# Performance work log

Measured on AMD Instinct MI355X. Metric: run time of the kernel, lower is better.

Reference implementation:

```python
import jax, jax.numpy as jnp
import numpy as np

B, N, D, HEAD = 16, 1024, 512, 256  # hidden_size=512, gcn_layer=2 -> head_dim=256


def _xavier(key, shape):
    lim = (6.0 / (shape[0] + shape[-1])) ** 0.5
    return jax.random.uniform(key, shape, jnp.float32, -lim, lim)


def setup_inputs() -> dict:
    key = jax.random.key(0)
    ks = jax.random.split(key, 10)
    fi_lim = (6.0 / (D + 1)) ** 0.5
    return {
        "x": jax.random.normal(ks[0], (B, N, D), jnp.float32),
        "tp_w": _xavier(ks[1], (D, D)), "tp_b": jnp.zeros((D,), jnp.float32),
        "tc_w": _xavier(ks[2], (D, D)), "tc_b": jnp.zeros((D,), jnp.float32),
        "fi_w": jax.random.uniform(ks[3], (D,), jnp.float32, -fi_lim, fi_lim),
        "bil_w": _xavier(ks[4], (D, D)),
        "gcn_w0": _xavier(ks[5], (D, HEAD)), "gcn_b0": jnp.zeros((HEAD,), jnp.float32),
        "gcn_w1": _xavier(ks[6], (D + HEAD, HEAD)), "gcn_b1": jnp.zeros((HEAD,), jnp.float32),
        "out_w": _xavier(ks[7], (D, D)), "out_b": jnp.zeros((D,), jnp.float32),
    }


def reference(x, tp_w, tp_b, tc_w, tc_b, fi_w, bil_w,
              gcn_w0, gcn_b0, gcn_w1, gcn_b1, out_w, out_b):
    Bb, Nn, Dd = x.shape
    # ---- StructInduction: matrix-tree latent structure ----
    tp = jnp.tanh(x @ tp_w + tp_b)                      # [B,N,D]
    tc = jnp.tanh(x @ tc_w + tc_b)                      # [B,N,D]
    # original expands BOTH tp and tc along dim 2 -> f_ij[b,i,j] = s[b,i]
    s = jnp.einsum('bnd,de,bne->bn', tp, bil_w, tc)     # [B,N]
    f_i = jnp.exp(x @ fi_w)                             # [B,N] root scores
    eye = jnp.eye(Nn, dtype=x.dtype)
    A = jnp.exp(s)[:, :, None] * (1.0 - eye)            # [B,N,N], zero diagonal
    col_sum = A.sum(axis=1)                             # [B,N] sum over dim 1
    L = -A + col_sum[:, None, :] * eye                  # Laplacian
    L = L.at[:, 0, :].set(f_i)                          # replace row 0 with root scores
    Linv = jnp.linalg.inv(L)                            # [B,N,N]
    d0 = f_i * Linv[:, :, 0]                            # [B,N]
    diag = jnp.diagonal(Linv, axis1=-2, axis2=-1)       # [B,N]
    tmp1 = A * diag[:, None, :]                         # A[b,i,j]*Linv_diag[b,j]
    tmp2 = A * jnp.swapaxes(Linv, 1, 2)                 # A[b,i,j]*Linv[b,j,i]
    mask1 = jnp.concatenate([jnp.zeros((Nn, 1), x.dtype),
                             jnp.ones((Nn, Nn - 1), x.dtype)], axis=1)  # zero col 0
    mask2 = mask1.T                                     # zero row 0
    dx = mask1 * tmp1 - mask2 * tmp2                    # [B,N,N]
    d = jnp.concatenate([d0[:, None, :], dx], axis=1)   # [B,N+1,N]
    df = jnp.swapaxes(d, 1, 2)                          # [B,N,N+1]
    adj = df[:, :, 1:]                                  # [B,N,N] latent adjacency
    # ---- GraphConvLayer (self_loop=True, dropout = identity / eval) ----
    denom = adj.sum(axis=2, keepdims=True) + 1.0        # [B,N,1]
    outputs = x
    cache = [x]
    outs = []
    for (W, b) in ((gcn_w0, gcn_b0), (gcn_w1, gcn_b1)):
        Ax = adj @ outputs                              # [B,N,in_dim]
        AxW = (Ax @ W + b) + (outputs @ W + b)          # neighbor + self loop
        g = jax.nn.relu(AxW / denom)                    # [B,N,HEAD]
        cache.append(g)
        outputs = jnp.concatenate(cache, axis=2)        # densely connected
        outs.append(g)
    gcn_out = jnp.concatenate(outs, axis=2) + x         # [B,N,D] residual
    return gcn_out @ out_w + out_b
```

## Files before the change

### kernel.cpp

```cpp
#include <hip/hip_runtime.h>
#include <cmath>

#define BN   16384
#define DD   512
#define HEADN 256

typedef unsigned short ushort;
typedef short short8 __attribute__((ext_vector_type(8)));
typedef float floatx4 __attribute__((ext_vector_type(4)));
typedef unsigned short ushort4v __attribute__((ext_vector_type(4)));
typedef unsigned short ushort8v __attribute__((ext_vector_type(8)));

__device__ __forceinline__ ushort f2bf(float v) {
    unsigned int u = __float_as_uint(v);
    unsigned int r = u + 0x7FFFu + ((u >> 16) & 1u);
    return (ushort)(r >> 16);
}
__device__ __forceinline__ float bf2f(ushort u) {
    return __uint_as_float(((unsigned int)u) << 16);
}
__device__ __forceinline__ float tanh_fast(float x) {
    float xc = fminf(fmaxf(x, -15.0f), 15.0f);
    float e = __expf(2.0f * xc);
    return (e - 1.0f) * __builtin_amdgcn_rcpf(e + 1.0f);
}

template <int TM, int TN, int KK, int EPI>
__global__ __launch_bounds__(256) void gemm_lds(
    const ushort* __restrict__ A, int lda,
    const ushort* __restrict__ Bt, int N,
    const float* __restrict__ bias,
    const float* __restrict__ denom,
    const ushort* __restrict__ tcb, int tcld,
    float* __restrict__ s_arr,
    void* __restrict__ Cout, int ldc,
    const ushort* __restrict__ xgb, int xoff, ushort* __restrict__ gout)
{
    constexpr int MI = TM / 32;
    constexpr int NI = TN / 32;
    constexpr int ROWS = TM + TN;
    constexpr int CPT = (ROWS * 8) / 256;
    constexpr int MT = 16384 / TM;
    constexpr int MT_PER_BAND = MT / 8;
    constexpr int NK = KK >> 6;
    static_assert(NK >= 2, "need >=2 K-iters for depth-2 pipeline");
    static_assert(CPT == 6, "vmcnt literal below assumes CPT==6");
    __shared__ ushort S[3 * ROWS * 64];

    const int g = blockIdx.x;
    const int band = g & 7, within = g >> 3;
    const int nt = within / MT_PER_BAND;
    const int mt = band * MT_PER_BAND + (within - nt * MT_PER_BAND);
    const int m0 = mt * TM, n0 = nt * TN;
    const int w = threadIdx.x >> 6, L = threadIdx.x & 63;
    const int wr0 = (w >> 1) * (TM / 2), wc0 = (w & 1) * (TN / 2);
    const int lrow = L & 15, quad = L >> 4;

    const ushort* gbase[CPT];
#pragma unroll
    for (int rr = 0; rr < CPT; ++rr) {
        const int chunk = rr * 256 + (w << 6) + L;
        const int row = chunk >> 3, slot = chunk & 7;
        const int ca = slot ^ ((row >> 1) & 7);
        gbase[rr] = (row < TM)
            ? A  + (size_t)(m0 + row) * lda    + (ca << 3)
            : Bt + (size_t)(n0 + row - TM) * KK + (ca << 3);
    }

    floatx4 zero4 = {0.0f, 0.0f, 0.0f, 0.0f};
    floatx4 acc[MI][NI];
#pragma unroll
    for (int i = 0; i < MI; ++i)
#pragma unroll
        for (int j = 0; j < NI; ++j) acc[i][j] = zero4;

    auto stage = [&](int buf, int k0) {
        ushort* Sd = S + buf * (ROWS * 64);
#pragma unroll
        for (int rr = 0; rr < CPT; ++rr) {
            __builtin_amdgcn_global_load_lds(
                (const __attribute__((address_space(1))) unsigned int*)(gbase[rr] + k0),
                (__attribute__((address_space(3))) unsigned int*)(Sd + (rr * 256 + (w << 6)) * 8),
                16, 0, 0);
        }
    };

    stage(0, 0);
    stage(1, 64);
#pragma unroll
    for (int kk = 0; kk < NK; ++kk) {
        if (kk + 1 < NK) {
            asm volatile("s_waitcnt vmcnt(6) lgkmcnt(0)" ::: "memory");
            __builtin_amdgcn_s_barrier();
            __builtin_amdgcn_sched_barrier(0);
        } else {
            __syncthreads();
        }
        if (kk + 2 < NK) stage((kk + 2) % 3, (kk + 2) << 6);

        const ushort* Sc = S + (kk % 3) * (ROWS * 64);
        short8 af[2][MI], bfr[2][NI];
#pragma unroll
        for (int ks = 0; ks < 2; ++ks) {
#pragma unroll
            for (int mi = 0; mi < MI; ++mi) {
                const int row = wr0 + (mi << 4) + lrow;
                const int slot = ((ks << 2) + quad) ^ ((row >> 1) & 7);
                af[ks][mi] = *(const short8*)(Sc + row * 64 + (slot << 3));
            }
#pragma unroll
            for (int ni = 0; ni < NI; ++ni) {
                const int row = TM + wc0 + (ni << 4) + lrow;
                const int slot = ((ks << 2) + quad) ^ ((row >> 1) & 7);
                bfr[ks][ni] = *(const short8*)(Sc + row * 64 + (slot << 3));
            }
        }
#pragma unroll
        for (int ks = 0; ks < 2; ++ks)
#pragma unroll
            for (int mi = 0; mi < MI; ++mi)
#pragma unroll
                for (int ni = 0; ni < NI; ++ni)
                    acc[mi][ni] = __builtin_amdgcn_mfma_f32_16x16x32_bf16(
                        bfr[ks][ni], af[ks][mi], acc[mi][ni], 0, 0, 0);
    }

    if constexpr (EPI == 3) {
#pragma unroll
        for (int mi = 0; mi < MI; ++mi) {
            const int gr = m0 + wr0 + (mi << 4) + lrow;
            float rs = 0.0f;
#pragma unroll
            for (int ni = 0; ni < NI; ++ni) {
                const int gcb = n0 + wc0 + (ni << 4) + (quad << 2);
                ushort4v t4 = *(const ushort4v*)(tcb + (size_t)gr * tcld + gcb);
#pragma unroll
                for (int p = 0; p < 4; ++p) rs += acc[mi][ni][p] * bf2f(t4[p]);
            }
            rs += __shfl_xor(rs, 16);
            rs += __shfl_xor(rs, 32);
            if (quad == 0) atomicAdd(s_arr + gr, rs);
        }
    } else {
#pragma unroll
        for (int mi = 0; mi < MI; ++mi) {
            const int gr = m0 + wr0 + (mi << 4) + lrow;
            const float rdv = (EPI == 2) ? __builtin_amdgcn_rcpf(denom[gr]) : 1.0f;
#pragma unroll
            for (int ni = 0; ni < NI; ++ni) {
                const int gcb = n0 + wc0 + (ni << 4) + (quad << 2);
                const floatx4 v = acc[mi][ni];
                if constexpr (EPI == 0) {
                    float4 bv = *(const float4*)(bias + gcb);
                    float4 o = {v[0] + bv.x, v[1] + bv.y, v[2] + bv.z, v[3] + bv.w};
                    *(float4*)((float*)Cout + (size_t)gr * ldc + gcb) = o;
                } else if constexpr (EPI == 1) {
                    float4 bv = *(const float4*)(bias + gcb);
                    ushort4v o;
                    o[0] = f2bf(tanh_fast(v[0] + bv.x));
                    o[1] = f2bf(tanh_fast(v[1] + bv.y));
                    o[2] = f2bf(tanh_fast(v[2] + bv.z));
                    o[3] = f2bf(tanh_fast(v[3] + bv.w));
                    *(ushort4v*)((ushort*)Cout + (size_t)gr * ldc + gcb) = o;
                } else {
                    float4 bv = *(const float4*)(bias + gcb);
                    float u0 = (v[0] + 2.0f * bv.x) * rdv; u0 = u0 > 0.0f ? u0 : 0.0f;
                    float u1 = (v[1] + 2.0f * bv.y) * rdv; u1 = u1 > 0.0f ? u1 : 0.0f;
                    float u2 = (v[2] + 2.0f * bv.z) * rdv; u2 = u2 > 0.0f ? u2 : 0.0f;
                    float u3 = (v[3] + 2.0f * bv.w) * rdv; u3 = u3 > 0.0f ? u3 : 0.0f;
                    if (Cout) {
                        ushort4v o;
                        o[0] = f2bf(u0); o[1] = f2bf(u1); o[2] = f2bf(u2); o[3] = f2bf(u3);
                        *(ushort4v*)((ushort*)Cout + (size_t)gr * ldc + gcb) = o;
                    }
                    if (gout) {
                        const size_t gb = (size_t)gr * 512 + xoff + gcb;
                        ushort4v xg = *(const ushort4v*)(xgb + gb);
                        ushort4v o;
                        o[0] = f2bf(u0 + bf2f(xg[0]));
                        o[1] = f2bf(u1 + bf2f(xg[1]));
                        o[2] = f2bf(u2 + bf2f(xg[2]));
                        o[3] = f2bf(u3 + bf2f(xg[3]));
                        *(ushort4v*)(gout + gb) = o;
                    }
                }
            }
        }
    }
}

__global__ __launch_bounds__(256) void prep_k(
    const float* __restrict__ x, const float* __restrict__ fiw,
    ushort* __restrict__ xb, float* __restrict__ fdot,
    const float* __restrict__ tp_w, const float* __restrict__ tc_w,
    const float* __restrict__ bilw, const float* __restrict__ ow,
    const float* __restrict__ w0, const float* __restrict__ w1,
    const float* __restrict__ tp_b, const float* __restrict__ tc_b,
    ushort* __restrict__ tptcwT, ushort* __restrict__ bilwT,
    ushort* __restrict__ owT, ushort* __restrict__ w0T,
    ushort* __restrict__ w1T, float* __restrict__ bias2,
    float* __restrict__ zstats, int zcount)
{
    const int blk0 = blockIdx.x;
    if (blk0 < 4096) {
        const int wv = threadIdx.x >> 6, L = threadIdx.x & 63;
        const int r = (blk0 << 2) + wv;
        const float* xr = x + (size_t)r * DD;
        const int c0 = L << 3;
        float4 v0 = *(const float4*)(xr + c0);
        float4 v1 = *(const float4*)(xr + c0 + 4);
        float4 f0 = *(const float4*)(fiw + c0);
        float4 f1 = *(const float4*)(fiw + c0 + 4);
        float d = v0.x * f0.x + v0.y * f0.y + v0.z * f0.z + v0.w * f0.w
                + v1.x * f1.x + v1.y * f1.y + v1.z * f1.z + v1.w * f1.w;
        ushort8v o;
        o[0] = f2bf(v0.x); o[1] = f2bf(v0.y); o[2] = f2bf(v0.z); o[3] = f2bf(v0.w);
        o[4] = f2bf(v1.x); o[5] = f2bf(v1.y); o[6] = f2bf(v1.z); o[7] = f2bf(v1.w);
        *(ushort8v*)(xb + (size_t)r * DD + c0) = o;
#pragma unroll
        for (int off = 32; off > 0; off >>= 1) d += __shfl_xor(d, off);
        if (L == 0) fdot[r] = d;
        return;
    }
    if (blk0 >= 5441) {
        for (int i = (blk0 - 5441) * 256 + threadIdx.x; i < zcount; i += 16 * 256)
            zstats[i] = 0.0f;
        return;
    }
    const int blk = blk0 - 4096;
    if (blk >= 1344) {
        for (int i = threadIdx.x; i < 512; i += 256) {
            bias2[i] = tp_b[i];
            bias2[512 + i] = tc_b[i];
        }
        return;
    }
    const float* W; ushort* Wt; int K, N, local;
    if (blk < 256)       { W = tp_w; Wt = tptcwT;              K = 512; N = 512; local = blk; }
    else if (blk < 512)  { W = tc_w; Wt = tptcwT + 512 * 512;  K = 512; N = 512; local = blk - 256; }
    else if (blk < 768)  { W = bilw; Wt = bilwT;               K = 512; N = 512; local = blk - 512; }
    else if (blk < 1024) { W = ow;   Wt = owT;                 K = 512; N = 512; local = blk - 768; }
    else if (blk < 1152) { W = w0;   Wt = w0T;                 K = 512; N = 256; local = blk - 1024; }
    else                 { W = w1;   Wt = w1T;                 K = 768; N = 256; local = blk - 1152; }

    __shared__ float t[32][33];
    const int nb = N >> 5;
    const int kb = local / nb, nbb = local % nb;
    const int k0 = kb << 5, n0 = nbb << 5;
    const int c = threadIdx.x & 31, r = threadIdx.x >> 5;
#pragma unroll
    for (int i = 0; i < 4; ++i)
        t[r + 8 * i][c] = W[(size_t)(k0 + r + 8 * i) * N + n0 + c];
    __syncthreads();
#pragma unroll
    for (int i = 0; i < 4; ++i)
        Wt[(size_t)(n0 + r + 8 * i) * K + k0 + c] = f2bf(t[c][r + 8 * i]);
}

__global__ __launch_bounds__(1024) void finalize_k(
    const float* __restrict__ s_arr, const float* __restrict__ fdot,
    float* __restrict__ a, float* __restrict__ f,
    float* __restrict__ Sb, float* __restrict__ Hb, float* __restrict__ den)
{
    __shared__ float redS[16], redH[16];
    __shared__ float Hsh;
    const int b = blockIdx.x, t = threadIdx.x;
    const int r = (b << 10) + t;
    const float av = __expf(s_arr[r]), fv = __expf(fdot[r]);
    a[r] = av; f[r] = fv;
    float s1 = av, s2 = av * fv;
#pragma unroll
    for (int o = 32; o > 0; o >>= 1) { s1 += __shfl_xor(s1, o); s2 += __shfl_xor(s2, o); }
    if ((t & 63) == 0) { redS[t >> 6] = s1; redH[t >> 6] = s2; }
    __syncthreads();
    if (t == 0) {
        float S = 0.f, H = 0.f;
        for (int i = 0; i < 16; ++i) { S += redS[i]; H += redH[i]; }
        Sb[b] = S; Hb[b] = H; Hsh = H;
    }
    __syncthreads();
    den[r] = 2.0f - av * fv * __builtin_amdgcn_rcpf(Hsh);
}

__global__ __launch_bounds__(256) void batch_pq(
    const ushort* __restrict__ V, const float* __restrict__ a, const float* __restrict__ f,
    float* __restrict__ P, float* __restrict__ Q, int C)
{
    __shared__ float redP[256][4];
    __shared__ float redQ[256][4];
    const int b = blockIdx.x >> 4;
    const int chunk = blockIdx.x & 15;
    const int c4cnt = C >> 2;
    const int rg = 256 / c4cnt;
    const int c4 = threadIdx.x & (c4cnt - 1);
    const int sub = threadIdx.x / c4cnt;
    const ushort* Vb = V + (size_t)b * 1024 * C;
    const float* ab = a + (b << 10);
    const float* fb = f + (b << 10);
    const int n0 = chunk << 6;
    float4 p = {0, 0, 0, 0}, q = {0, 0, 0, 0};
    for (int n = n0 + sub; n < n0 + 64; n += rg) {
        const float av = ab[n], afv = av * fb[n];
        ushort4v u = *(const ushort4v*)(Vb + (size_t)n * C + (c4 << 2));
        float4 v = {bf2f(u[0]), bf2f(u[1]), bf2f(u[2]), bf2f(u[3])};
        p.x += av * v.x; p.y += av * v.y; p.z += av * v.z; p.w += av * v.w;
        q.x += afv * v.x; q.y += afv * v.y; q.z += afv * v.z; q.w += afv * v.w;
    }
    redP[threadIdx.x][0] = p.x; redP[threadIdx.x][1] = p.y;
    redP[threadIdx.x][2] = p.z; redP[threadIdx.x][3] = p.w;
    redQ[threadIdx.x][0] = q.x; redQ[threadIdx.x][1] = q.y;
    redQ[threadIdx.x][2] = q.z; redQ[threadIdx.x][3] = q.w;
    __syncthreads();
    if (sub == 0) {
        for (int s = 1; s < rg; ++s) {
            const int t2 = threadIdx.x + s * c4cnt;
            p.x += redP[t2][0]; p.y += redP[t2][1]; p.z += redP[t2][2]; p.w += redP[t2][3];
            q.x += redQ[t2][0]; q.y += redQ[t2][1]; q.z += redQ[t2][2]; q.w += redQ[t2][3];
        }
        float* Pp = P + b * C + (c4 << 2);
        float* Qp = Q + b * C + (c4 << 2);
        atomicAdd(Pp + 0, p.x); atomicAdd(Pp + 1, p.y);
        atomicAdd(Pp + 2, p.z); atomicAdd(Pp + 3, p.w);
        atomicAdd(Qp + 0, q.x); atomicAdd(Qp + 1, q.y);
        atomicAdd(Qp + 2, q.z); atomicAdd(Qp + 3, q.w);
    }
}

__global__ __launch_bounds__(256) void mix_k(
    const ushort* __restrict__ V, const float* __restrict__ P, const float* __restrict__ Q,
    const float* __restrict__ a, const float* __restrict__ f,
    const float* __restrict__ Sb, const float* __restrict__ Hb,
    ushort* __restrict__ outb, int C, int ldo, int co)
{
    const int idx = blockIdx.x * 256 + threadIdx.x;
    const int c4c = C >> 2;
    const int r = idx / c4c, c4 = idx - r * c4c;
    const int b = r >> 10;
    const float av = a[r], fv = f[r], S = Sb[b], H = Hb[b];
    const float rS = __builtin_amdgcn_rcpf(S);
    const float beta = av * rS * __builtin_amdgcn_rcpf(H);
    const float alpha = 1.0f - av * rS;
    const float cp = rS - beta * fv;
    ushort4v u = *(const ushort4v*)(V + (size_t)r * C + (c4 << 2));
    float4 v = {bf2f(u[0]), bf2f(u[1]), bf2f(u[2]), bf2f(u[3])};
    const float* Pp = P + b * C + (c4 << 2);
    const float* Qp = Q + b * C + (c4 << 2);
    ushort4v o;
    o[0] = f2bf(alpha * v.x + cp * Pp[0] + beta * Qp[0]);
    o[1] = f2bf(alpha * v.y + cp * Pp[1] + beta * Qp[1]);
    o[2] = f2bf(alpha * v.z + cp * Pp[2] + beta * Qp[2]);
    o[3] = f2bf(alpha * v.w + cp * Pp[3] + beta * Qp[3]);
    *(ushort4v*)(outb + (size_t)r * ldo + co + (c4 << 2)) = o;
}

extern "C" void kernel_launch(void* const* d_in, const int* in_sizes, int n_in,
                              void* d_out, int out_size, void* d_ws, size_t ws_size,
                              hipStream_t stream)
{
    (void)in_sizes; (void)n_in; (void)out_size; (void)ws_size;
    const float* x    = (const float*)d_in[0];
    const float* tp_w = (const float*)d_in[1];
    const float* tp_b = (const float*)d_in[2];
    const float* tc_w = (const float*)d_in[3];
    const float* tc_b = (const float*)d_in[4];
    const float* fi_w = (const float*)d_in[5];
    const float* bilw = (const float*)d_in[6];
    const float* w0   = (const float*)d_in[7];
    const float* b0   = (const float*)d_in[8];
    const float* w1   = (const float*)d_in[9];
    const float* b1   = (const float*)d_in[10];
    const float* ow   = (const float*)d_in[11];
    const float* ob   = (const float*)d_in[12];

    char* W = (char*)d_ws;
    ushort* xb    = (ushort*)W;
    ushort* gcnb  = xb;
    ushort* tptcb = (ushort*)(W + ((size_t)16 << 20));
    ushort* Hbuf  = tptcb;
    ushort* g0b   = (ushort*)(W + ((size_t)48 << 20));
    ushort* tptcwT= (ushort*)(W + ((size_t)56 << 20));
    ushort* bilwT = tptcwT + 524288;
    ushort* owT   = bilwT + 262144;
    ushort* w0T   = owT + 262144;
    ushort* w1T   = w0T + 131072;
    float*  bias2 = (float*)(w1T + 196608);
    float* stats  = (float*)(W + ((size_t)60 << 20));
    float* s_arr  = stats;
    float* P0     = s_arr + 16384;
    float* Q0     = P0 + 8192;
    float* P1     = Q0 + 8192;
    float* Q1     = P1 + 4096;
    const int zcount = 16384 + 2 * 8192 + 2 * 4096;
    float* fdot   = Q1 + 4096;
    float* arr_a  = fdot + BN;
    float* arr_f  = arr_a + BN;
    float* arr_den= arr_f + BN;
    float* Sb     = arr_den + BN;
    float* Hb     = Sb + 16;

    prep_k<<<5457, 256, 0, stream>>>(x, fi_w, xb, fdot, tp_w, tc_w, bilw, ow, w0, w1,
                                     tp_b, tc_b, tptcwT, bilwT, owT, w0T, w1T, bias2,
                                     s_arr, zcount);
    gemm_lds<128, 64, 512, 1><<<2048, 256, 0, stream>>>(xb, 512, tptcwT, 1024, bias2,
        nullptr, nullptr, 0, nullptr, tptcb, 1024, nullptr, 0, nullptr);
    gemm_lds<128, 64, 512, 3><<<1024, 256, 0, stream>>>(tptcb, 1024, bilwT, 512, nullptr,
        nullptr, tptcb + 512, 1024, s_arr, nullptr, 0, nullptr, 0, nullptr);
    finalize_k<<<16, 1024, 0, stream>>>(s_arr, fdot, arr_a, arr_f, Sb, Hb, arr_den);
    batch_pq<<<256, 256, 0, stream>>>(xb, arr_a, arr_f, P0, Q0, 512);
    mix_k<<<8192, 256, 0, stream>>>(xb, P0, Q0, arr_a, arr_f, Sb, Hb, Hbuf, 512, 768, 0);
    gemm_lds<128, 64, 512, 2><<<512, 256, 0, stream>>>(Hbuf, 768, w0T, 256, b0,
        arr_den, nullptr, 0, nullptr, g0b, 256, xb, 0, gcnb);
    batch_pq<<<256, 256, 0, stream>>>(g0b, arr_a, arr_f, P1, Q1, 256);
    mix_k<<<4096, 256, 0, stream>>>(g0b, P1, Q1, arr_a, arr_f, Sb, Hb, Hbuf, 256, 768, 512);
    gemm_lds<128, 64, 768, 2><<<512, 256, 0, stream>>>(Hbuf, 768, w1T, 256, b1,
        arr_den, nullptr, 0, nullptr, nullptr, 0, xb, 256, gcnb);
    gemm_lds<128, 64, 512, 0><<<1024, 256, 0, stream>>>(gcnb, 512, owT, 512, ob,
        nullptr, nullptr, 0, nullptr, (float*)d_out, 512, nullptr, 0, nullptr);
}
```

Before: 230.8 us.

## Fuse finalize into batch_pq and fold layer-1 P/Q reduction into GEMM epilogue

Removes the separate finalize kernel by computing exp of scores, per-batch sums S and H (via atomics) inside the first batch-reduction kernel, and computing the denominator in the mix kernel. The second batch_pq launch is eliminated by accumulating the weighted column sums P1/Q1 directly in the layer-0 GEMM epilogue with shuffle reductions and atomics. This cuts two launches and a re-read of g0b, at the cost of extra atomics and register pressure in the GEMM epilogue and slight numeric differences from summing unrounded values.

After: 236.7 us. 1.03x slower.

```diff
diff --git a/kernel.cpp b/kernel.cpp
--- a/kernel.cpp
+++ b/kernel.cpp
@@ -34,7 +34,9 @@
     const ushort* __restrict__ tcb, int tcld,
     float* __restrict__ s_arr,
     void* __restrict__ Cout, int ldc,
-    const ushort* __restrict__ xgb, int xoff, ushort* __restrict__ gout)
+    const ushort* __restrict__ xgb, int xoff, ushort* __restrict__ gout,
+    const float* __restrict__ pq_a, const float* __restrict__ pq_f,
+    float* __restrict__ Pq, float* __restrict__ Qq)
 {
     constexpr int MI = TM / 32;
     constexpr int NI = TN / 32;
@@ -142,10 +144,20 @@
             if (quad == 0) atomicAdd(s_arr + gr, rs);
         }
     } else {
+        float sP[NI][4], sQ[NI][4];
+        if constexpr (EPI == 4) {
+#pragma unroll
+            for (int ni = 0; ni < NI; ++ni)
+#pragma unroll
+                for (int p = 0; p < 4; ++p) { sP[ni][p] = 0.f; sQ[ni][p] = 0.f; }
+        }
 #pragma unroll
         for (int mi = 0; mi < MI; ++mi) {
             const int gr = m0 + wr0 + (mi << 4) + lrow;
-            const float rdv = (EPI == 2) ? __builtin_amdgcn_rcpf(denom[gr]) : 1.0f;
+            const float rdv = (EPI == 2 || EPI == 4)
+                            ? __builtin_amdgcn_rcpf(denom[gr]) : 1.0f;
+            float av_r = 0.f, afv_r = 0.f;
+            if constexpr (EPI == 4) { av_r = pq_a[gr]; afv_r = av_r * pq_f[gr]; }
 #pragma unroll
             for (int ni = 0; ni < NI; ++ni) {
                 const int gcb = n0 + wc0 + (ni << 4) + (quad << 2);
@@ -183,6 +195,32 @@
                         o[3] = f2bf(u3 + bf2f(xg[3]));
                         *(ushort4v*)(gout + gb) = o;
                     }
+                    if constexpr (EPI == 4) {
+                        sP[ni][0] += av_r * u0;  sQ[ni][0] += afv_r * u0;
+                        sP[ni][1] += av_r * u1;  sQ[ni][1] += afv_r * u1;
+                        sP[ni][2] += av_r * u2;  sQ[ni][2] += afv_r * u2;
+                        sP[ni][3] += av_r * u3;  sQ[ni][3] += afv_r * u3;
+                    }
+                }
+            }
+        }
+        if constexpr (EPI == 4) {
+            const int bb = m0 >> 10;
+#pragma unroll
+            for (int ni = 0; ni < NI; ++ni) {
+                const int gcb = n0 + wc0 + (ni << 4) + (quad << 2);
+#pragma unroll
+                for (int p = 0; p < 4; ++p) {
+                    float vP = sP[ni][p], vQ = sQ[ni][p];
+#pragma unroll
+                    for (int o = 1; o < 16; o <<= 1) {
+                        vP += __shfl_xor(vP, o);
+                        vQ += __shfl_xor(vQ, o);
+                    }
+                    if (lrow == 0) {
+                        atomicAdd(Pq + bb * HEADN + gcb + p, vP);
+                        atomicAdd(Qq + bb * HEADN + gcb + p, vQ);
+                    }
                 }
             }
         }
@@ -257,37 +295,16 @@
         Wt[(size_t)(n0 + r + 8 * i) * K + k0 + c] = f2bf(t[c][r + 8 * i]);
 }
 
-__global__ __launch_bounds__(1024) void finalize_k(
-    const float* __restrict__ s_arr, const float* __restrict__ fdot,
+__global__ __launch_bounds__(256) void batch_pq_f(
+    const ushort* __restrict__ V, const float* __restrict__ s_arr,
+    const float* __restrict__ fdot,
     float* __restrict__ a, float* __restrict__ f,
-    float* __restrict__ Sb, float* __restrict__ Hb, float* __restrict__ den)
-{
-    __shared__ float redS[16], redH[16];
-    __shared__ float Hsh;
-    const int b = blockIdx.x, t = threadIdx.x;
-    const int r = (b << 10) + t;
-    const float av = __expf(s_arr[r]), fv = __expf(fdot[r]);
-    a[r] = av; f[r] = fv;
-    float s1 = av, s2 = av * fv;
-#pragma unroll
-    for (int o = 32; o > 0; o >>= 1) { s1 += __shfl_xor(s1, o); s2 += __shfl_xor(s2, o); }
-    if ((t & 63) == 0) { redS[t >> 6] = s1; redH[t >> 6] = s2; }
-    __syncthreads();
-    if (t == 0) {
-        float S = 0.f, H = 0.f;
-        for (int i = 0; i < 16; ++i) { S += redS[i]; H += redH[i]; }
-        Sb[b] = S; Hb[b] = H; Hsh = H;
-    }
-    __syncthreads();
-    den[r] = 2.0f - av * fv * __builtin_amdgcn_rcpf(Hsh);
-}
-
-__global__ __launch_bounds__(256) void batch_pq(
-    const ushort* __restrict__ V, const float* __restrict__ a, const float* __restrict__ f,
-    float* __restrict__ P, float* __restrict__ Q, int C)
+    float* __restrict__ P, float* __restrict__ Q,
+    float* __restrict__ Sb, float* __restrict__ Hb, int C)
 {
     __shared__ float redP[256][4];
     __shared__ float redQ[256][4];
+    __shared__ float sSh[4], sHh[4];
     const int b = blockIdx.x >> 4;
     const int chunk = blockIdx.x & 15;
     const int c4cnt = C >> 2;
@@ -295,22 +312,37 @@
     const int c4 = threadIdx.x & (c4cnt - 1);
     const int sub = threadIdx.x / c4cnt;
     const ushort* Vb = V + (size_t)b * 1024 * C;
-    const float* ab = a + (b << 10);
-    const float* fb = f + (b << 10);
+    const float* sB = s_arr + (b << 10);
+    const float* fB = fdot + (b << 10);
     const int n0 = chunk << 6;
     float4 p = {0, 0, 0, 0}, q = {0, 0, 0, 0};
+    float sS = 0.f, sH = 0.f;
     for (int n = n0 + sub; n < n0 + 64; n += rg) {
-        const float av = ab[n], afv = av * fb[n];
+        const float av = __expf(sB[n]);
+        const float fv = __expf(fB[n]);
+        const float afv = av * fv;
+        if (c4 == 0) {
+            a[(b << 10) + n] = av;
+            f[(b << 10) + n] = fv;
+            sS += av; sH += afv;
+        }
         ushort4v u = *(const ushort4v*)(Vb + (size_t)n * C + (c4 << 2));
         float4 v = {bf2f(u[0]), bf2f(u[1]), bf2f(u[2]), bf2f(u[3])};
         p.x += av * v.x; p.y += av * v.y; p.z += av * v.z; p.w += av * v.w;
         q.x += afv * v.x; q.y += afv * v.y; q.z += afv * v.z; q.w += afv * v.w;
     }
+    if (c4 == 0) { sSh[sub] = sS; sHh[sub] = sH; }
     redP[threadIdx.x][0] = p.x; redP[threadIdx.x][1] = p.y;
     redP[threadIdx.x][2] = p.z; redP[threadIdx.x][3] = p.w;
     redQ[threadIdx.x][0] = q.x; redQ[threadIdx.x][1] = q.y;
     redQ[threadIdx.x][2] = q.z; redQ[threadIdx.x][3] = q.w;
     __syncthreads();
+    if (threadIdx.x == 0) {
+        float tS = 0.f, tH = 0.f;
+        for (int s = 0; s < rg; ++s) { tS += sSh[s]; tH += sHh[s]; }
+        atomicAdd(Sb + b, tS);
+        atomicAdd(Hb + b, tH);
+    }
     if (sub == 0) {
         for (int s = 1; s < rg; ++s) {
             const int t2 = threadIdx.x + s * c4cnt;
@@ -330,7 +362,8 @@
     const ushort* __restrict__ V, const float* __restrict__ P, const float* __restrict__ Q,
     const float* __restrict__ a, const float* __restrict__ f,
     const float* __restrict__ Sb, const float* __restrict__ Hb,
-    ushort* __restrict__ outb, int C, int ldo, int co)
+    ushort* __restrict__ outb, int C, int ldo, int co,
+    float* __restrict__ den)
 {
     const int idx = blockIdx.x * 256 + threadIdx.x;
     const int c4c = C >> 2;
@@ -338,9 +371,11 @@
     const int b = r >> 10;
     const float av = a[r], fv = f[r], S = Sb[b], H = Hb[b];
     const float rS = __builtin_amdgcn_rcpf(S);
-    const float beta = av * rS * __builtin_amdgcn_rcpf(H);
+    const float rH = __builtin_amdgcn_rcpf(H);
+    const float beta = av * rS * rH;
     const float alpha = 1.0f - av * rS;
     const float cp = rS - beta * fv;
+    if (den && c4 == 0) den[r] = 2.0f - av * fv * rH;
     ushort4v u = *(const ushort4v*)(V + (size_t)r * C + (c4 << 2));
     float4 v = {bf2f(u[0]), bf2f(u[1]), bf2f(u[2]), bf2f(u[3])};
     const float* Pp = P + b * C + (c4 << 2);
@@ -390,30 +425,36 @@
     float* Q0     = P0 + 8192;
     float* P1     = Q0 + 8192;
     float* Q1     = P1 + 4096;
-    const int zcount = 16384 + 2 * 8192 + 2 * 4096;
-    float* fdot   = Q1 + 4096;
+    float* Sb     = Q1 + 4096;
+    float* Hb     = Sb + 16;
+    const int zcount = 16384 + 2 * 8192 + 2 * 4096 + 32;
+    float* fdot   = Hb + 16;
     float* arr_a  = fdot + BN;
     float* arr_f  = arr_a + BN;
     float* arr_den= arr_f + BN;
-    float* Sb     = arr_den + BN;
-    float* Hb     = Sb + 16;
 
     prep_k<<<5457, 256, 0, stream>>>(x, fi_w, xb, fdot, tp_w, tc_w, bilw, ow, w0, w1,
                                      tp_b, tc_b, tptcwT, bilwT, owT, w0T, w1T, bias2,
                                      s_arr, zcount);
     gemm_lds<128, 64, 512, 1><<<2048, 256, 0, stream>>>(xb, 512, tptcwT, 1024, bias2,
-        nullptr, nullptr, 0, nullptr, tptcb, 1024, nullptr, 0, nullptr);
+        nullptr, nullptr, 0, nullptr, tptcb, 1024, nullptr, 0, nullptr,
+        nullptr, nullptr, nullptr, nullptr);
     gemm_lds<128, 64, 512, 3><<<1024, 256, 0, stream>>>(tptcb, 1024, bilwT, 512, nullptr,
-        nullptr, tptcb + 512, 1024, s_arr, nullptr, 0, nullptr, 0, nullptr);
-    finalize_k<<<16, 1024, 0, stream>>>(s_arr, fdot, arr_a, arr_f, Sb, Hb, arr_den);
-    batch_pq<<<256, 256, 0, stream>>>(xb, arr_a, arr_f, P0, Q0, 512);
-    mix_k<<<8192, 256, 0, stream>>>(xb, P0, Q0, arr_a, arr_f, Sb, Hb, Hbuf, 512, 768, 0);
-    gemm_lds<128, 64, 512, 2><<<512, 256, 0, stream>>>(Hbuf, 768, w0T, 256, b0,
-        arr_den, nullptr, 0, nullptr, g0b, 256, xb, 0, gcnb);
-    batch_pq<<<256, 256, 0, stream>>>(g0b, arr_a, arr_f, P1, Q1, 256);
-    mix_k<<<4096, 256, 0, stream>>>(g0b, P1, Q1, arr_a, arr_f, Sb, Hb, Hbuf, 256, 768, 512);
+        nullptr, tptcb + 512, 1024, s_arr, nullptr, 0, nullptr, 0, nullptr,
+        nullptr, nullptr, nullptr, nullptr);
+    batch_pq_f<<<256, 256, 0, stream>>>(xb, s_arr, fdot, arr_a, arr_f,
+                                        P0, Q0, Sb, Hb, 512);
+    mix_k<<<8192, 256, 0, stream>>>(xb, P0, Q0, arr_a, arr_f, Sb, Hb,
+                                    Hbuf, 512, 768, 0, arr_den);
+    gemm_lds<128, 64, 512, 4><<<512, 256, 0, stream>>>(Hbuf, 768, w0T, 256, b0,
+        arr_den, nullptr, 0, nullptr, g0b, 256, xb, 0, gcnb,
+        arr_a, arr_f, P1, Q1);
+    mix_k<<<4096, 256, 0, stream>>>(g0b, P1, Q1, arr_a, arr_f, Sb, Hb,
+                                    Hbuf, 256, 768, 512, nullptr);
     gemm_lds<128, 64, 768, 2><<<512, 256, 0, stream>>>(Hbuf, 768, w1T, 256, b1,
-        arr_den, nullptr, 0, nullptr, nullptr, 0, xb, 256, gcnb);
+        arr_den, nullptr, 0, nullptr, nullptr, 0, xb, 256, gcnb,
+        nullptr, nullptr, nullptr, nullptr);
     gemm_lds<128, 64, 512, 0><<<1024, 256, 0, stream>>>(gcnb, 512, owT, 512, ob,
-        nullptr, nullptr, 0, nullptr, (float*)d_out, 512, nullptr, 0, nullptr);
-}
+        nullptr, nullptr, 0, nullptr, (float*)d_out, 512, nullptr, 0, nullptr,
+        nullptr, nullptr, nullptr, nullptr);
+}
```

## Add double-buffered 128x128 GEMM kernel with async LDS loads for three GEMMs

Applied to the files above, without the earlier changes.

Adds a new GEMM kernel with 128x128 tiles that double-buffers 64-wide K slices into LDS using global_load_lds, XOR-swizzled layout, and explicit waitcnt/barrier scheduling with priority bumps around the MFMA block. It replaces the projection GEMM, the bilinear score GEMM and the output GEMM, halving grid sizes because the tile N doubles. It also remaps block indices into M bands so neighbouring blocks share A rows. The goal is to overlap global loads with MFMA work and get more reuse per tile, at the cost of more registers and LDS per block, which may lower occupancy.

New measurement: 225.4 us. 1.02x faster.

```diff
diff --git a/kernel.cpp b/kernel.cpp
--- a/kernel.cpp
+++ b/kernel.cpp
@@ -189,6 +189,150 @@
     }
 }
 
+template <int KK, int EPI>
+__global__ __launch_bounds__(256) void gemm2p(
+    const ushort* __restrict__ A, int lda,
+    const ushort* __restrict__ Bt, int N,
+    const float* __restrict__ bias,
+    const ushort* __restrict__ tcb, int tcld,
+    float* __restrict__ s_arr,
+    void* __restrict__ Cout, int ldc)
+{
+    constexpr int TM = 128, TN = 128;
+    constexpr int MI = 4, NI = 4;
+    constexpr int ROWS = 256;
+    constexpr int CPT = 8;
+    constexpr int MT = 128, MT_PER_BAND = 16;
+    constexpr int NK = KK >> 6;
+    static_assert(NK >= 2, "pipeline needs >=2 K-iters");
+    __shared__ ushort S[2 * ROWS * 64];
+
+    const int g = blockIdx.x;
+    const int band = g & 7, within = g >> 3;
+    const int nt = within / MT_PER_BAND;
+    const int mt = band * MT_PER_BAND + (within - nt * MT_PER_BAND);
+    const int m0 = mt * TM, n0 = nt * TN;
+    const int w = threadIdx.x >> 6, L = threadIdx.x & 63;
+    const int wr0 = (w >> 1) * 64, wc0 = (w & 1) * 64;
+    const int lrow = L & 15, quad = L >> 4;
+
+    const ushort* gbase[CPT];
+#pragma unroll
+    for (int rr = 0; rr < CPT; ++rr) {
+        const int chunk = rr * 256 + (w << 6) + L;
+        const int row = chunk >> 3, slot = chunk & 7;
+        const int ca = slot ^ ((row >> 1) & 7);
+        gbase[rr] = (row < TM)
+            ? A  + (size_t)(m0 + row) * lda    + (ca << 3)
+            : Bt + (size_t)(n0 + row - TM) * KK + (ca << 3);
+    }
+
+    floatx4 zero4 = {0.0f, 0.0f, 0.0f, 0.0f};
+    floatx4 acc[MI][NI];
+#pragma unroll
+    for (int i = 0; i < MI; ++i)
+#pragma unroll
+        for (int j = 0; j < NI; ++j) acc[i][j] = zero4;
+
+    auto stage = [&](int buf, int k0) {
+        ushort* Sd = S + buf * (ROWS * 64);
+#pragma unroll
+        for (int rr = 0; rr < CPT; ++rr) {
+            __builtin_amdgcn_global_load_lds(
+                (const __attribute__((address_space(1))) unsigned int*)(gbase[rr] + k0),
+                (__attribute__((address_space(3))) unsigned int*)(Sd + (rr * 256 + (w << 6)) * 8),
+                16, 0, 0);
+        }
+    };
+
+    stage(0, 0);
+    stage(1, 64);
+#pragma unroll
+    for (int kk = 0; kk < NK; ++kk) {
+        if (kk + 1 < NK)
+            asm volatile("s_waitcnt vmcnt(8) lgkmcnt(0)" ::: "memory");
+        else
+            asm volatile("s_waitcnt vmcnt(0) lgkmcnt(0)" ::: "memory");
+        __builtin_amdgcn_s_barrier();
+        __builtin_amdgcn_sched_barrier(0);
+
+        const ushort* Sc = S + (kk & 1) * (ROWS * 64);
+        short8 af[2][MI], bfr[2][NI];
+#pragma unroll
+        for (int ks = 0; ks < 2; ++ks) {
+#pragma unroll
+            for (int mi = 0; mi < MI; ++mi) {
+                const int row = wr0 + (mi << 4) + lrow;
+                const int slot = ((ks << 2) + quad) ^ ((row >> 1) & 7);
+                af[ks][mi] = *(const short8*)(Sc + row * 64 + (slot << 3));
+            }
+#pragma unroll
+            for (int ni = 0; ni < NI; ++ni) {
+                const int row = TM + wc0 + (ni << 4) + lrow;
+                const int slot = ((ks << 2) + quad) ^ ((row >> 1) & 7);
+                bfr[ks][ni] = *(const short8*)(Sc + row * 64 + (slot << 3));
+            }
+        }
+        asm volatile("s_waitcnt lgkmcnt(0)" ::: "memory");
+        __builtin_amdgcn_sched_barrier(0);
+        __builtin_amdgcn_s_barrier();
+        __builtin_amdgcn_sched_barrier(0);
+        if (kk + 2 < NK) stage(kk & 1, (kk + 2) << 6);
+
+        __builtin_amdgcn_s_setprio(1);
+#pragma unroll
+        for (int ks = 0; ks < 2; ++ks)
+#pragma unroll
+            for (int mi = 0; mi < MI; ++mi)
+#pragma unroll
+                for (int ni = 0; ni < NI; ++ni)
+                    acc[mi][ni] = __builtin_amdgcn_mfma_f32_16x16x32_bf16(
+                        bfr[ks][ni], af[ks][mi], acc[mi][ni], 0, 0, 0);
+        __builtin_amdgcn_s_setprio(0);
+    }
+
+    if constexpr (EPI == 3) {
+#pragma unroll
+        for (int mi = 0; mi < MI; ++mi) {
+            const int gr = m0 + wr0 + (mi << 4) + lrow;
+            float rs = 0.0f;
+#pragma unroll
+            for (int ni = 0; ni < NI; ++ni) {
+                const int gcb = n0 + wc0 + (ni << 4) + (quad << 2);
+                ushort4v t4 = *(const ushort4v*)(tcb + (size_t)gr * tcld + gcb);
+#pragma unroll
+                for (int p = 0; p < 4; ++p) rs += acc[mi][ni][p] * bf2f(t4[p]);
+            }
+            rs += __shfl_xor(rs, 16);
+            rs += __shfl_xor(rs, 32);
+            if (quad == 0) atomicAdd(s_arr + gr, rs);
+        }
+    } else {
+#pragma unroll
+        for (int mi = 0; mi < MI; ++mi) {
+            const int gr = m0 + wr0 + (mi << 4) + lrow;
+#pragma unroll
+            for (int ni = 0; ni < NI; ++ni) {
+                const int gcb = n0 + wc0 + (ni << 4) + (quad << 2);
+                const floatx4 v = acc[mi][ni];
+                if constexpr (EPI == 0) {
+                    float4 bv = *(const float4*)(bias + gcb);
+                    float4 o = {v[0] + bv.x, v[1] + bv.y, v[2] + bv.z, v[3] + bv.w};
+                    *(float4*)((float*)Cout + (size_t)gr * ldc + gcb) = o;
+                } else {
+                    float4 bv = *(const float4*)(bias + gcb);
+                    ushort4v o;
+                    o[0] = f2bf(tanh_fast(v[0] + bv.x));
+                    o[1] = f2bf(tanh_fast(v[1] + bv.y));
+                    o[2] = f2bf(tanh_fast(v[2] + bv.z));
+                    o[3] = f2bf(tanh_fast(v[3] + bv.w));
+                    *(ushort4v*)((ushort*)Cout + (size_t)gr * ldc + gcb) = o;
+                }
+            }
+        }
+    }
+}
+
 __global__ __launch_bounds__(256) void prep_k(
     const float* __restrict__ x, const float* __restrict__ fiw,
     ushort* __restrict__ xb, float* __restrict__ fdot,
@@ -401,10 +545,10 @@
     prep_k<<<5457, 256, 0, stream>>>(x, fi_w, xb, fdot, tp_w, tc_w, bilw, ow, w0, w1,
                                      tp_b, tc_b, tptcwT, bilwT, owT, w0T, w1T, bias2,
                                      s_arr, zcount);
-    gemm_lds<128, 64, 512, 1><<<2048, 256, 0, stream>>>(xb, 512, tptcwT, 1024, bias2,
-        nullptr, nullptr, 0, nullptr, tptcb, 1024, nullptr, 0, nullptr);
-    gemm_lds<128, 64, 512, 3><<<1024, 256, 0, stream>>>(tptcb, 1024, bilwT, 512, nullptr,
-        nullptr, tptcb + 512, 1024, s_arr, nullptr, 0, nullptr, 0, nullptr);
+    gemm2p<512, 1><<<1024, 256, 0, stream>>>(xb, 512, tptcwT, 1024, bias2,
+        nullptr, 0, nullptr, tptcb, 1024);
+    gemm2p<512, 3><<<512, 256, 0, stream>>>(tptcb, 1024, bilwT, 512, nullptr,
+        tptcb + 512, 1024, s_arr, nullptr, 0);
     finalize_k<<<16, 1024, 0, stream>>>(s_arr, fdot, arr_a, arr_f, Sb, Hb, arr_den);
     batch_pq<<<256, 256, 0, stream>>>(xb, arr_a, arr_f, P0, Q0, 512);
     mix_k<<<8192, 256, 0, stream>>>(xb, P0, Q0, arr_a, arr_f, Sb, Hb, Hbuf, 512, 768, 0);
@@ -414,6 +558,6 @@
     mix_k<<<4096, 256, 0, stream>>>(g0b, P1, Q1, arr_a, arr_f, Sb, Hb, Hbuf, 256, 768, 512);
     gemm_lds<128, 64, 768, 2><<<512, 256, 0, stream>>>(Hbuf, 768, w1T, 256, b1,
         arr_den, nullptr, 0, nullptr, nullptr, 0, xb, 256, gcnb);
-    gemm_lds<128, 64, 512, 0><<<1024, 256, 0, stream>>>(gcnb, 512, owT, 512, ob,
-        nullptr, nullptr, 0, nullptr, (float*)d_out, 512, nullptr, 0, nullptr);
-}
+    gemm2p<512, 0><<<512, 256, 0, stream>>>(gcnb, 512, owT, 512, ob,
+        nullptr, 0, nullptr, (float*)d_out, 512);
+}
```

## Switch GEMM to double-buffered LDS pipeline with larger 128x128 tiles

Applied to the files above, without the earlier changes.

The GEMM kernel moves from a three-buffer LDS ring to two buffers. Each K-step now reads fragments into registers first, then issues the next stage's global-to-LDS loads into the buffer just freed, and raises wave priority around the MFMA block. The tp/tc, bilinear and output projections now use 128x128 tiles with half as many blocks, for more reuse per LDS load. The trade-off is an extra barrier per iteration and larger tiles that may lower occupancy or raise register pressure.

New measurement: 232.6 us. About the same (+0.8%).

```diff
diff --git a/kernel.cpp b/kernel.cpp
--- a/kernel.cpp
+++ b/kernel.cpp
@@ -26,7 +26,7 @@
 }
 
 template <int TM, int TN, int KK, int EPI>
-__global__ __launch_bounds__(256) void gemm_lds(
+__global__ __launch_bounds__(256) void gemm2p(
     const ushort* __restrict__ A, int lda,
     const ushort* __restrict__ Bt, int N,
     const float* __restrict__ bias,
@@ -43,9 +43,9 @@
     constexpr int MT = 16384 / TM;
     constexpr int MT_PER_BAND = MT / 8;
     constexpr int NK = KK >> 6;
-    static_assert(NK >= 2, "need >=2 K-iters for depth-2 pipeline");
-    static_assert(CPT == 6, "vmcnt literal below assumes CPT==6");
-    __shared__ ushort S[3 * ROWS * 64];
+    static_assert(NK >= 2, "pipeline needs >=2 K-iters");
+    static_assert(CPT == 6 || CPT == 8, "vmcnt literal dispatch");
+    __shared__ ushort S[2 * ROWS * 64];
 
     const int g = blockIdx.x;
     const int band = g & 7, within = g >> 3;
@@ -90,15 +90,17 @@
 #pragma unroll
     for (int kk = 0; kk < NK; ++kk) {
         if (kk + 1 < NK) {
-            asm volatile("s_waitcnt vmcnt(6) lgkmcnt(0)" ::: "memory");
-            __builtin_amdgcn_s_barrier();
-            __builtin_amdgcn_sched_barrier(0);
+            if constexpr (CPT == 6)
+                asm volatile("s_waitcnt vmcnt(6) lgkmcnt(0)" ::: "memory");
+            else
+                asm volatile("s_waitcnt vmcnt(8) lgkmcnt(0)" ::: "memory");
         } else {
-            __syncthreads();
-        }
-        if (kk + 2 < NK) stage((kk + 2) % 3, (kk + 2) << 6);
-
-        const ushort* Sc = S + (kk % 3) * (ROWS * 64);
+            asm volatile("s_waitcnt vmcnt(0) lgkmcnt(0)" ::: "memory");
+        }
+        __builtin_amdgcn_s_barrier();
+        __builtin_amdgcn_sched_barrier(0);
+
+        const ushort* Sc = S + (kk & 1) * (ROWS * 64);
         short8 af[2][MI], bfr[2][NI];
 #pragma unroll
         for (int ks = 0; ks < 2; ++ks) {
@@ -115,6 +117,13 @@
                 bfr[ks][ni] = *(const short8*)(Sc + row * 64 + (slot << 3));
             }
         }
+        asm volatile("s_waitcnt lgkmcnt(0)" ::: "memory");
+        __builtin_amdgcn_sched_barrier(0);
+        __builtin_amdgcn_s_barrier();
+        __builtin_amdgcn_sched_barrier(0);
+        if (kk + 2 < NK) stage(kk & 1, (kk + 2) << 6);
+
+        __builtin_amdgcn_s_setprio(1);
 #pragma unroll
         for (int ks = 0; ks < 2; ++ks)
 #pragma unroll
@@ -123,6 +132,7 @@
                 for (int ni = 0; ni < NI; ++ni)
                     acc[mi][ni] = __builtin_amdgcn_mfma_f32_16x16x32_bf16(
                         bfr[ks][ni], af[ks][mi], acc[mi][ni], 0, 0, 0);
+        __builtin_amdgcn_s_setprio(0);
     }
 
     if constexpr (EPI == 3) {
@@ -401,19 +411,19 @@
     prep_k<<<5457, 256, 0, stream>>>(x, fi_w, xb, fdot, tp_w, tc_w, bilw, ow, w0, w1,
                                      tp_b, tc_b, tptcwT, bilwT, owT, w0T, w1T, bias2,
                                      s_arr, zcount);
-    gemm_lds<128, 64, 512, 1><<<2048, 256, 0, stream>>>(xb, 512, tptcwT, 1024, bias2,
+    gemm2p<128, 128, 512, 1><<<1024, 256, 0, stream>>>(xb, 512, tptcwT, 1024, bias2,
         nullptr, nullptr, 0, nullptr, tptcb, 1024, nullptr, 0, nullptr);
-    gemm_lds<128, 64, 512, 3><<<1024, 256, 0, stream>>>(tptcb, 1024, bilwT, 512, nullptr,
+    gemm2p<128, 128, 512, 3><<<512, 256, 0, stream>>>(tptcb, 1024, bilwT, 512, nullptr,
         nullptr, tptcb + 512, 1024, s_arr, nullptr, 0, nullptr, 0, nullptr);
     finalize_k<<<16, 1024, 0, stream>>>(s_arr, fdot, arr_a, arr_f, Sb, Hb, arr_den);
     batch_pq<<<256, 256, 0, stream>>>(xb, arr_a, arr_f, P0, Q0, 512);
     mix_k<<<8192, 256, 0, stream>>>(xb, P0, Q0, arr_a, arr_f, Sb, Hb, Hbuf, 512, 768, 0);
-    gemm_lds<128, 64, 512, 2><<<512, 256, 0, stream>>>(Hbuf, 768, w0T, 256, b0,
+    gemm2p<128, 64, 512, 2><<<512, 256, 0, stream>>>(Hbuf, 768, w0T, 256, b0,
         arr_den, nullptr, 0, nullptr, g0b, 256, xb, 0, gcnb);
     batch_pq<<<256, 256, 0, stream>>>(g0b, arr_a, arr_f, P1, Q1, 256);
     mix_k<<<4096, 256, 0, stream>>>(g0b, P1, Q1, arr_a, arr_f, Sb, Hb, Hbuf, 256, 768, 512);
-    gemm_lds<128, 64, 768, 2><<<512, 256, 0, stream>>>(Hbuf, 768, w1T, 256, b1,
+    gemm2p<128, 64, 768, 2><<<512, 256, 0, stream>>>(Hbuf, 768, w1T, 256, b1,
         arr_den, nullptr, 0, nullptr, nullptr, 0, xb, 256, gcnb);
-    gemm_lds<128, 64, 512, 0><<<1024, 256, 0, stream>>>(gcnb, 512, owT, 512, ob,
+    gemm2p<128, 128, 512, 0><<<512, 256, 0, stream>>>(gcnb, 512, owT, 512, ob,
         nullptr, nullptr, 0, nullptr, (float*)d_out, 512, nullptr, 0, nullptr);
 }
```
